# Performance work log

Hardware: AMD Instinct MI355X
Metric: run time of the kernel (lower is better)

Reference implementation:

```python
import math
import jax
import jax.numpy as jnp
import numpy as np

DIM = 1024
NUM_EXPERTS = 4
CAPACITY = (0.25, 0.25, 0.25, 0.25)
BATCH = 8
NUM_TOKENS = 4096


def setup_inputs() -> dict:
    key = jax.random.key(0)
    k1, k2 = jax.random.split(key)
    input_tokens = jax.random.normal(k1, (BATCH, NUM_TOKENS, DIM), dtype=jnp.float32)
    # torch Linear weight [out_features, in_features], init uniform(-0.02, 0.02), bias zeros
    W = jax.random.uniform(k2, (NUM_EXPERTS, DIM), dtype=jnp.float32, minval=-0.02, maxval=0.02)
    b = jnp.zeros((NUM_EXPERTS,), dtype=jnp.float32)
    return {"input_tokens": input_tokens, "W": W, "b": b}


def reference(input_tokens, W, b):
    # router probs in float32 (autocast disabled in original)
    logits = jnp.einsum('bnd,ed->bne', input_tokens, W) + b  # [B, N, E]
    probs = jax.nn.softmax(logits, axis=-1)

    B, N, _ = probs.shape
    token_mask = jnp.full((B, N), -1, dtype=jnp.int32)
    neg_inf = jnp.float32(-jnp.inf)

    # Sequential expert-preferred assignment, highest expert index first.
    for j in reversed(range(NUM_EXPERTS)):
        capacity = int(math.floor(CAPACITY[j] * N))
        if capacity == 0:
            continue
        r_j = jnp.where(token_mask != -1, neg_inf, probs[:, :, j])  # mask already-assigned tokens
        _, topk_idx = jax.lax.top_k(r_j, capacity)  # [B, capacity]
        # Faithful to torch `token_mask[:, topk_indices] = j`: assigns expert j at the
        # union of selected token positions across ALL batch rows (broadcast over dim 0).
        token_mask = token_mask.at[:, topk_idx.reshape(-1)].set(j)

    token_mask = jnp.where(token_mask == -1, 0, token_mask)
    expert_probs = jnp.take_along_axis(probs, token_mask[..., None], axis=2)[..., 0]  # [B, N]
    return token_mask, expert_probs
```

## Files before the change

### kernel.cpp

```cpp
#include <hip/hip_runtime.h>
#include <math.h>

#define DIM 1024
#define NE 4
#define NTOK 4096
#define NB 8
#define CAP 1024

__global__ __launch_bounds__(256) void probs_kernel(const float* __restrict__ tokens,
                                                    const float* __restrict__ W,
                                                    const float* __restrict__ bias,
                                                    float* __restrict__ probs) {
    __shared__ float4 Wl[NE * 256];
    int tid = threadIdx.x;
    const float4* W4 = (const float4*)W;
    for (int i = tid; i < NE * 256; i += 256) Wl[i] = W4[i];
    __syncthreads();

    int wave = tid >> 6, lane = tid & 63;
    long tok = (long)blockIdx.x * 4 + wave;
    const float4* t4 = (const float4*)(tokens + tok * DIM);

    double a0 = 0, a1 = 0, a2 = 0, a3 = 0;
#pragma unroll
    for (int kk = 0; kk < 4; kk++) {
        int c = lane + 64 * kk;
        float4 v  = t4[c];
        float4 w0 = Wl[0 * 256 + c];
        float4 w1 = Wl[1 * 256 + c];
        float4 w2 = Wl[2 * 256 + c];
        float4 w3 = Wl[3 * 256 + c];
        a0 += (double)v.x * w0.x + (double)v.y * w0.y + (double)v.z * w0.z + (double)v.w * w0.w;
        a1 += (double)v.x * w1.x + (double)v.y * w1.y + (double)v.z * w1.z + (double)v.w * w1.w;
        a2 += (double)v.x * w2.x + (double)v.y * w2.y + (double)v.z * w2.z + (double)v.w * w2.w;
        a3 += (double)v.x * w3.x + (double)v.y * w3.y + (double)v.z * w3.z + (double)v.w * w3.w;
    }
#pragma unroll
    for (int off = 32; off > 0; off >>= 1) {
        a0 += __shfl_xor(a0, off);
        a1 += __shfl_xor(a1, off);
        a2 += __shfl_xor(a2, off);
        a3 += __shfl_xor(a3, off);
    }
    if (lane == 0) {
        float f0 = (float)(a0 + (double)bias[0]);
        float f1 = (float)(a1 + (double)bias[1]);
        float f2 = (float)(a2 + (double)bias[2]);
        float f3 = (float)(a3 + (double)bias[3]);
        double m = fmax(fmax((double)f0, (double)f1), fmax((double)f2, (double)f3));
        double e0 = exp((double)f0 - m);
        double e1 = exp((double)f1 - m);
        double e2 = exp((double)f2 - m);
        double e3 = exp((double)f3 - m);
        double s = e0 + e1 + e2 + e3;
        float4 p;
        p.x = (float)(e0 / s);
        p.y = (float)(e1 / s);
        p.z = (float)(e2 / s);
        p.w = (float)(e3 / s);
        ((float4*)probs)[tok] = p;
    }
}


__device__ __forceinline__ unsigned block_exscan_1024(unsigned v, unsigned* wl,
                                                      int tid, unsigned* total) {
    int lane = tid & 63, w = tid >> 6;
    unsigned s = v;
#pragma unroll
    for (int off = 1; off < 64; off <<= 1) {
        unsigned t = __shfl_up(s, off);
        if (lane >= off) s += t;
    }
    if (lane == 63) wl[w] = s;
    __syncthreads();
    if (tid < 64) {
        unsigned x = (tid < 16) ? wl[tid] : 0u;
#pragma unroll
        for (int off = 1; off < 16; off <<= 1) {
            unsigned t = __shfl_up(x, off);
            if (lane >= off) x += t;
        }
        if (tid < 16) wl[tid] = x;
    }
    __syncthreads();
    unsigned waveoff = (w == 0) ? 0u : wl[w - 1];
    unsigned tot = wl[15];
    __syncthreads();
    if (total) *total = tot;
    return waveoff + (s - v);
}

__device__ __forceinline__ void radix_select_1024(const unsigned* keys, unsigned cap,
                                                  unsigned* hist, unsigned* scanb,
                                                  unsigned* bcast, int tid,
                                                  unsigned* v_out, unsigned* rem_out) {
    if (tid == 0) { bcast[0] = 0u; bcast[1] = cap; }
    __syncthreads();
#pragma unroll
    for (int shift = 24; shift >= 0; shift -= 8) {
        if (tid < 256) hist[tid] = 0u;
        __syncthreads();
        unsigned pref = bcast[0], rem = bcast[1];
        bool all = (shift == 24);
#pragma unroll
        for (int k = 0; k < 4; k++) {
            unsigned K = keys[tid + k * 1024];
            if (all || (K >> (shift + 8)) == pref)
                atomicAdd(&hist[(K >> shift) & 255u], 1u);
        }
        __syncthreads();
        if (tid < 64) {
            unsigned h0 = hist[4 * tid], h1 = hist[4 * tid + 1];
            unsigned h2 = hist[4 * tid + 2], h3 = hist[4 * tid + 3];
            unsigned s3 = h3, s2 = h2 + s3, s1 = h1 + s2, s0 = h0 + s1;
            unsigned t = s0, s = t;
#pragma unroll
            for (int off = 1; off < 64; off <<= 1) {
                unsigned o = __shfl_down(s, off);
                if (tid + off < 64) s += o;
            }
            unsigned E = s - t;
            scanb[4 * tid]     = E + s0;
            scanb[4 * tid + 1] = E + s1;
            scanb[4 * tid + 2] = E + s2;
            scanb[4 * tid + 3] = E + s3;
        }
        __syncthreads();
        if (tid < 256) {
            unsigned incl = scanb[tid];
            unsigned excl = (tid < 255) ? scanb[tid + 1] : 0u;
            if (excl < rem && rem <= incl) {
                bcast[0] = (pref << 8) | (unsigned)tid;
                bcast[1] = rem - excl;
            }
        }
        __syncthreads();
    }
    *v_out = bcast[0];
    *rem_out = bcast[1];
}

__device__ __forceinline__ unsigned mono_key(float p) {
    unsigned bits = __float_as_uint(p);
    return (bits & 0x80000000u) ? ~bits : (bits | 0x80000000u);
}

__global__ __launch_bounds__(1024) void select3_kernel(const float* __restrict__ probs,
                                                       unsigned* __restrict__ selbits) {
    __shared__ unsigned keys[NTOK];
    __shared__ unsigned hist[256], scanb[256], bcast[2];
    __shared__ unsigned bitmap[128];
    __shared__ unsigned wl[17];
    int b = blockIdx.x, tid = threadIdx.x;

#pragma unroll
    for (int k = 0; k < 4; k++) {
        int i = tid + k * 1024;
        keys[i] = mono_key(probs[((size_t)b * NTOK + i) * NE + 3]);
    }
    if (tid < 128) bitmap[tid] = 0u;
    __syncthreads();

    unsigned vstar, rem;
    radix_select_1024(keys, CAP, hist, scanb, bcast, tid, &vstar, &rem);

    unsigned loc[4], v = 0;
#pragma unroll
    for (int k = 0; k < 4; k++) { loc[k] = (keys[4 * tid + k] == vstar); v += loc[k]; }
    unsigned tot;
    unsigned ex = block_exscan_1024(v, wl, tid, &tot);
#pragma unroll
    for (int k = 0; k < 4; k++) {
        int i = 4 * tid + k;
        bool sel = (keys[i] > vstar) || (loc[k] && ex < rem);
        ex += loc[k];
        if (sel) atomicOr(&bitmap[i >> 5], 1u << (i & 31));
    }
    __syncthreads();
    if (tid < 128) selbits[b * 128 + tid] = bitmap[tid];
}

__global__ __launch_bounds__(1024) void rest_kernel(const float* __restrict__ probs,
                                                    const unsigned* __restrict__ selbits,
                                                    int* __restrict__ finalmask) {
    __shared__ unsigned keys[NTOK];
    __shared__ int maskv[NTOK];
    __shared__ unsigned hist[256], scanb[256], bcast[2];
    __shared__ unsigned bitmap[128];
    __shared__ unsigned wl[17];
    int tid = threadIdx.x;

    if (tid < 128) {
        unsigned u = 0;
#pragma unroll
        for (int b = 0; b < NB; b++) u |= selbits[b * 128 + tid];
        bitmap[tid] = u;
    }
    __syncthreads();
#pragma unroll
    for (int k = 0; k < 4; k++) {
        int i = tid + k * 1024;
        maskv[i] = ((bitmap[i >> 5] >> (i & 31)) & 1u) ? 3 : -1;
    }
    __syncthreads();

    for (int j = 2; j >= 0; j--) {
        unsigned loc[4], v = 0;
#pragma unroll
        for (int k = 0; k < 4; k++) { loc[k] = (maskv[4 * tid + k] != -1); v += loc[k]; }
        unsigned M;
        unsigned ex = block_exscan_1024(v, wl, tid, &M);
        unsigned U = NTOK - M;

        if (U <= CAP) {
            unsigned need = CAP - U;
#pragma unroll
            for (int k = 0; k < 4; k++) {
                int i = 4 * tid + k;
                bool sel = (!loc[k]) || (ex < need);
                ex += loc[k];
                if (sel) maskv[i] = j;
            }
            __syncthreads();
        } else {
            if (tid < 128) bitmap[tid] = 0u;
            __syncthreads();
            for (int b = 0; b < NB; b++) {
#pragma unroll
                for (int k = 0; k < 4; k++) {
                    int i = tid + k * 1024;
                    keys[i] = (maskv[i] != -1)
                                  ? 0u
                                  : mono_key(probs[((size_t)b * NTOK + i) * NE + j]);
                }
                __syncthreads();
                unsigned vstar, rem;
                radix_select_1024(keys, CAP, hist, scanb, bcast, tid, &vstar, &rem);
                unsigned l2[4], v2 = 0;
#pragma unroll
                for (int k = 0; k < 4; k++) { l2[k] = (keys[4 * tid + k] == vstar); v2 += l2[k]; }
                unsigned tot2;
                unsigned ex2 = block_exscan_1024(v2, wl, tid, &tot2);
#pragma unroll
                for (int k = 0; k < 4; k++) {
                    int i = 4 * tid + k;
                    bool sel = (keys[i] > vstar) || (l2[k] && ex2 < rem);
                    ex2 += l2[k];
                    if (sel) atomicOr(&bitmap[i >> 5], 1u << (i & 31));
                }
                __syncthreads();
            }
#pragma unroll
            for (int k = 0; k < 4; k++) {
                int i = 4 * tid + k;
                if ((bitmap[i >> 5] >> (i & 31)) & 1u) maskv[i] = j;
            }
            __syncthreads();
        }
    }

#pragma unroll
    for (int k = 0; k < 4; k++) {
        int i = tid + k * 1024;
        int m = maskv[i];
        finalmask[i] = (m < 0) ? 0 : m;
    }
}

__global__ __launch_bounds__(256) void final_kernel(const float* __restrict__ probs,
                                                    const int* __restrict__ fm,
                                                    float* __restrict__ out) {
    int i = blockIdx.x * 256 + threadIdx.x;
    int n = i & (NTOK - 1);
    int m = fm[n];
    out[i] = (float)m;
    out[NB * NTOK + i] = probs[(size_t)i * NE + m];
}

extern "C" void kernel_launch(void* const* d_in, const int* in_sizes, int n_in,
                              void* d_out, int out_size, void* d_ws, size_t ws_size,
                              hipStream_t stream) {
    const float* tokens = (const float*)d_in[0];
    const float* W      = (const float*)d_in[1];
    const float* bias   = (const float*)d_in[2];
    float* out = (float*)d_out;

    float*    probs   = (float*)d_ws;
    unsigned* selbits = (unsigned*)((char*)d_ws + (size_t)NB * NTOK * NE * sizeof(float));
    int*      fmask   = (int*)(selbits + NB * 128);

    probs_kernel<<<(NB * NTOK) / 4, 256, 0, stream>>>(tokens, W, bias, probs);
    select3_kernel<<<NB, 1024, 0, stream>>>(probs, selbits);
    rest_kernel<<<1, 1024, 0, stream>>>(probs, selbits, fmask);
    final_kernel<<<(NB * NTOK) / 256, 256, 0, stream>>>(probs, fmask, out);
}
```

Before: 208.8 us.

## Fuse select and rest kernels with last-block counter, keep radix keys in registers

Merges the per-batch expert-3 selection kernel and the single-block remaining-experts kernel into one launch. The last block to finish, found through an atomic counter reset in probs_kernel, carries out the sequential passes. Radix-select keys now live in registers instead of a shared-memory array, and the expert-3 probabilities are read as float4 with a contiguous per-thread layout. This removes one kernel launch and some shared-memory traffic, but relies on atomics and threadfence for cross-block visibility.

```diff
diff --git a/kernel.cpp b/kernel.cpp
--- a/kernel.cpp
+++ b/kernel.cpp
@@ -10,9 +10,11 @@
 __global__ __launch_bounds__(256) void probs_kernel(const float* __restrict__ tokens,
                                                     const float* __restrict__ W,
                                                     const float* __restrict__ bias,
-                                                    float* __restrict__ probs) {
+                                                    float* __restrict__ probs,
+                                                    unsigned* __restrict__ counter) {
     __shared__ float4 Wl[NE * 256];
     int tid = threadIdx.x;
+    if (blockIdx.x == 0 && tid == 0) counter[0] = 0u;
     const float4* W4 = (const float4*)W;
     for (int i = tid; i < NE * 256; i += 256) Wl[i] = W4[i];
     __syncthreads();
@@ -91,7 +93,7 @@
     return waveoff + (s - v);
 }
 
-__device__ __forceinline__ void radix_select_1024(const unsigned* keys, unsigned cap,
+__device__ __forceinline__ void radix_select_regs(const unsigned key[4], unsigned cap,
                                                   unsigned* hist, unsigned* scanb,
                                                   unsigned* bcast, int tid,
                                                   unsigned* v_out, unsigned* rem_out) {
@@ -105,9 +107,8 @@
         bool all = (shift == 24);
 #pragma unroll
         for (int k = 0; k < 4; k++) {
-            unsigned K = keys[tid + k * 1024];
-            if (all || (K >> (shift + 8)) == pref)
-                atomicAdd(&hist[(K >> shift) & 255u], 1u);
+            if (all || (key[k] >> (shift + 8)) == pref)
+                atomicAdd(&hist[(key[k] >> shift) & 255u], 1u);
         }
         __syncthreads();
         if (tid < 64) {
@@ -146,55 +147,58 @@
     return (bits & 0x80000000u) ? ~bits : (bits | 0x80000000u);
 }
 
-__global__ __launch_bounds__(1024) void select3_kernel(const float* __restrict__ probs,
-                                                       unsigned* __restrict__ selbits) {
-    __shared__ unsigned keys[NTOK];
-    __shared__ unsigned hist[256], scanb[256], bcast[2];
-    __shared__ unsigned bitmap[128];
-    __shared__ unsigned wl[17];
-    int b = blockIdx.x, tid = threadIdx.x;
-
-#pragma unroll
-    for (int k = 0; k < 4; k++) {
-        int i = tid + k * 1024;
-        keys[i] = mono_key(probs[((size_t)b * NTOK + i) * NE + 3]);
-    }
-    if (tid < 128) bitmap[tid] = 0u;
-    __syncthreads();
-
+__device__ __forceinline__ void select_to_bitmap(const unsigned key[4], unsigned* bitmap,
+                                                 unsigned* hist, unsigned* scanb,
+                                                 unsigned* bcast, unsigned* wl, int tid) {
     unsigned vstar, rem;
-    radix_select_1024(keys, CAP, hist, scanb, bcast, tid, &vstar, &rem);
-
+    radix_select_regs(key, CAP, hist, scanb, bcast, tid, &vstar, &rem);
     unsigned loc[4], v = 0;
 #pragma unroll
-    for (int k = 0; k < 4; k++) { loc[k] = (keys[4 * tid + k] == vstar); v += loc[k]; }
+    for (int k = 0; k < 4; k++) { loc[k] = (key[k] == vstar); v += loc[k]; }
     unsigned tot;
     unsigned ex = block_exscan_1024(v, wl, tid, &tot);
 #pragma unroll
     for (int k = 0; k < 4; k++) {
         int i = 4 * tid + k;
-        bool sel = (keys[i] > vstar) || (loc[k] && ex < rem);
+        bool sel = (key[k] > vstar) || (loc[k] && ex < rem);
         ex += loc[k];
         if (sel) atomicOr(&bitmap[i >> 5], 1u << (i & 31));
     }
     __syncthreads();
-    if (tid < 128) selbits[b * 128 + tid] = bitmap[tid];
-}
-
-__global__ __launch_bounds__(1024) void rest_kernel(const float* __restrict__ probs,
-                                                    const unsigned* __restrict__ selbits,
-                                                    int* __restrict__ finalmask) {
-    __shared__ unsigned keys[NTOK];
+}
+
+__global__ __launch_bounds__(1024) void selrest_kernel(const float* __restrict__ probs,
+                                                       unsigned* __restrict__ selbits,
+                                                       unsigned* __restrict__ counter,
+                                                       int* __restrict__ finalmask) {
     __shared__ int maskv[NTOK];
     __shared__ unsigned hist[256], scanb[256], bcast[2];
     __shared__ unsigned bitmap[128];
     __shared__ unsigned wl[17];
-    int tid = threadIdx.x;
-
+    __shared__ int islast;
+    int b = blockIdx.x, tid = threadIdx.x;
+
+    const float4* p4 = (const float4*)probs + (size_t)b * NTOK;
+    unsigned key[4];
+#pragma unroll
+    for (int k = 0; k < 4; k++) key[k] = mono_key(p4[4 * tid + k].w);
+    if (tid < 128) bitmap[tid] = 0u;
+    __syncthreads();
+
+    select_to_bitmap(key, bitmap, hist, scanb, bcast, wl, tid);
+
+    if (tid < 128) atomicExch(&selbits[b * 128 + tid], bitmap[tid]);
+    __threadfence();
+    __syncthreads();
+    if (tid == 0) islast = (atomicAdd(counter, 1u) == NB - 1);
+    __syncthreads();
+    if (!islast) return;
+
+    __threadfence();
     if (tid < 128) {
         unsigned u = 0;
 #pragma unroll
-        for (int b = 0; b < NB; b++) u |= selbits[b * 128 + tid];
+        for (int bb = 0; bb < NB; bb++) u |= atomicOr(&selbits[bb * 128 + tid], 0u);
         bitmap[tid] = u;
     }
     __syncthreads();
@@ -226,30 +230,16 @@
         } else {
             if (tid < 128) bitmap[tid] = 0u;
             __syncthreads();
-            for (int b = 0; b < NB; b++) {
-#pragma unroll
-                for (int k = 0; k < 4; k++) {
-                    int i = tid + k * 1024;
-                    keys[i] = (maskv[i] != -1)
-                                  ? 0u
-                                  : mono_key(probs[((size_t)b * NTOK + i) * NE + j]);
-                }
-                __syncthreads();
-                unsigned vstar, rem;
-                radix_select_1024(keys, CAP, hist, scanb, bcast, tid, &vstar, &rem);
-                unsigned l2[4], v2 = 0;
-#pragma unroll
-                for (int k = 0; k < 4; k++) { l2[k] = (keys[4 * tid + k] == vstar); v2 += l2[k]; }
-                unsigned tot2;
-                unsigned ex2 = block_exscan_1024(v2, wl, tid, &tot2);
+            for (int bb = 0; bb < NB; bb++) {
+                unsigned k2[4];
 #pragma unroll
                 for (int k = 0; k < 4; k++) {
                     int i = 4 * tid + k;
-                    bool sel = (keys[i] > vstar) || (l2[k] && ex2 < rem);
-                    ex2 += l2[k];
-                    if (sel) atomicOr(&bitmap[i >> 5], 1u << (i & 31));
+                    k2[k] = (maskv[i] != -1)
+                                ? 0u
+                                : mono_key(probs[((size_t)bb * NTOK + i) * NE + j]);
                 }
-                __syncthreads();
+                select_to_bitmap(k2, bitmap, hist, scanb, bcast, wl, tid);
             }
 #pragma unroll
             for (int k = 0; k < 4; k++) {
@@ -289,9 +279,9 @@
     float*    probs   = (float*)d_ws;
     unsigned* selbits = (unsigned*)((char*)d_ws + (size_t)NB * NTOK * NE * sizeof(float));
     int*      fmask   = (int*)(selbits + NB * 128);
-
-    probs_kernel<<<(NB * NTOK) / 4, 256, 0, stream>>>(tokens, W, bias, probs);
-    select3_kernel<<<NB, 1024, 0, stream>>>(probs, selbits);
-    rest_kernel<<<1, 1024, 0, stream>>>(probs, selbits, fmask);
+    unsigned* counter = (unsigned*)(fmask + NTOK);
+
+    probs_kernel<<<(NB * NTOK) / 4, 256, 0, stream>>>(tokens, W, bias, probs, counter);
+    selrest_kernel<<<NB, 1024, 0, stream>>>(probs, selbits, counter, fmask);
     final_kernel<<<(NB * NTOK) / 256, 256, 0, stream>>>(probs, fmask, out);
 }
```

Result: slower. 214.4 us (+2.7%).
